# Optimization experiments

Hardware: AMD Instinct MI355X
Metric: run time of the kernel (lower is better)

## Reference

```python
import jax, jax.numpy as jnp
import numpy as np

T = 2048            # context_length
C = 1024            # embedding size
HEAD_QK = 256       # config.head_qk_size
VOCAB = 50257       # config.vocab_size


def setup_inputs() -> dict:
    key = jax.random.key(0)
    k1, k2, k3, k4 = jax.random.split(key, 4)
    x = jax.random.normal(k1, (T, C), dtype=jnp.float32)
    idx = jax.random.randint(k2, (T,), 0, VOCAB, dtype=jnp.int32)
    # Dense kernels (flax Dense stores kernel as [in, out], no bias)
    Wq = jax.random.normal(k3, (C, HEAD_QK), dtype=jnp.float32) / np.sqrt(C)
    Wk = jax.random.normal(k4, (C, HEAD_QK), dtype=jnp.float32) / np.sqrt(C)
    return {"x": x, "idx": idx, "Wq": Wq, "Wk": Wk}


def reference(x, idx, Wq, Wk):
    # q, k: [T, HEAD_QK]
    q = x @ Wq
    k = x @ Wk
    # causal-masked, softmax-free scores: [T, T]
    c = (q @ k.T) * (1.0 / HEAD_QK)
    causal = jnp.tril(jnp.ones((T, T), dtype=bool))
    c = jnp.where(causal, c, 0.0)
    # c @ one_hot(idx, VOCAB) == segment-sum of c's columns by token id
    # out[t, v] = sum_{s : idx[s] == v} c[t, s]   -> [T, VOCAB]
    out = jax.ops.segment_sum(c.T, idx, num_segments=VOCAB).T
    return out
```

## Files before the change

### kernel.cpp

```cpp
#include <hip/hip_runtime.h>

#define T_CTX 2048
#define C_DIM 1024
#define HQK   256
#define NVOC  50257

typedef float nfloat4 __attribute__((ext_vector_type(4)));

__global__ __launch_bounds__(1024) void k_build_first(const int* __restrict__ idx,
                                                      int* __restrict__ first,
                                                      int* __restrict__ vocab_map) {
    __shared__ int sidx[T_CTX];
    __shared__ int skey[4096];
    __shared__ int sval[4096];
    const int tid = threadIdx.x;
    for (int i = tid; i < T_CTX; i += 1024) sidx[i] = idx[i];
    for (int i = tid; i < 4096; i += 1024) { skey[i] = -1; sval[i] = 0x7fffffff; }
    int4* vm4 = reinterpret_cast<int4*>(vocab_map);
    const int4 neg1 = make_int4(-1, -1, -1, -1);
    for (int i = tid; i < 12564; i += 1024) vm4[i] = neg1;
    if (tid == 0) vocab_map[NVOC - 1] = -1;
    __syncthreads();
#pragma unroll
    for (int rep = 0; rep < 2; ++rep) {
        const int s = tid + rep * 1024;
        const int my = sidx[s];
        int h = (int)(((unsigned)my * 2654435761u) >> 16) & 4095;
        while (true) {
            int k = skey[h];
            if (k == my) break;
            if (k == -1) {
                int old = atomicCAS(&skey[h], -1, my);
                if (old == -1 || old == my) break;
            }
            h = (h + 1) & 4095;
        }
        atomicMin(&sval[h], s);
    }
    __syncthreads();
#pragma unroll
    for (int rep = 0; rep < 2; ++rep) {
        const int s = tid + rep * 1024;
        const int my = sidx[s];
        int h = (int)(((unsigned)my * 2654435761u) >> 16) & 4095;
        while (skey[h] != my) h = (h + 1) & 4095;
        const int mp = sval[h];
        first[s] = mp;
        if (mp == s) vocab_map[my] = s;
    }
}

__global__ __launch_bounds__(512) void k_gemm_qk(const float* __restrict__ x,
                                                 const float* __restrict__ Wq,
                                                 const float* __restrict__ Wk,
                                                 float* __restrict__ qbuf,
                                                 float* __restrict__ kT) {
    __shared__ __align__(16) float As[32 * 68];
    __shared__ __align__(16) float Bs[32 * 68];
    const int row0 = blockIdx.x * 64;
    const int col0 = blockIdx.y * 64;
    const bool is_q = (col0 < HQK);
    const float* __restrict__ W = is_q ? Wq : Wk;
    const int wc0 = is_q ? col0 : (col0 - HQK);
    const int tid = threadIdx.x;
    const int tr = (tid >> 4) << 1;
    const int tc = (tid & 15) << 2;
    const int ar = tid >> 3, ak = (tid & 7) << 2;
    const int bk = tid >> 4, bc = (tid & 15) << 2;
    float acc[2][4] = {};
    for (int k0 = 0; k0 < C_DIM; k0 += 32) {
        float4 a4 = *reinterpret_cast<const float4*>(&x[(size_t)(row0 + ar) * C_DIM + k0 + ak]);
        float4 b4 = *reinterpret_cast<const float4*>(&W[(size_t)(k0 + bk) * HQK + wc0 + bc]);
        As[(ak + 0) * 68 + ar] = a4.x; As[(ak + 1) * 68 + ar] = a4.y;
        As[(ak + 2) * 68 + ar] = a4.z; As[(ak + 3) * 68 + ar] = a4.w;
        *reinterpret_cast<float4*>(&Bs[bk * 68 + bc]) = b4;
        __syncthreads();
#pragma unroll
        for (int kk = 0; kk < 32; ++kk) {
            float2 av = *reinterpret_cast<const float2*>(&As[kk * 68 + tr]);
            float4 bv = *reinterpret_cast<const float4*>(&Bs[kk * 68 + tc]);
            const float a[2] = {av.x, av.y};
            const float b[4] = {bv.x, bv.y, bv.z, bv.w};
#pragma unroll
            for (int i = 0; i < 2; ++i)
#pragma unroll
                for (int j = 0; j < 4; ++j) acc[i][j] = fmaf(a[i], b[j], acc[i][j]);
        }
        __syncthreads();
    }
    if (is_q) {
#pragma unroll
        for (int i = 0; i < 2; ++i) {
            float4 o = {acc[i][0], acc[i][1], acc[i][2], acc[i][3]};
            *reinterpret_cast<float4*>(&qbuf[(size_t)(row0 + tr + i) * HQK + col0 + tc]) = o;
        }
    } else {
#pragma unroll
        for (int j = 0; j < 4; ++j) {
            float2 o = {acc[0][j], acc[1][j]};
            *reinterpret_cast<float2*>(&kT[(size_t)(wc0 + tc + j) * T_CTX + row0 + tr]) = o;
        }
    }
}

__global__ __launch_bounds__(512) void k_scores_gemm(const float* __restrict__ q,
                                                     const float* __restrict__ kT,
                                                     float* __restrict__ c) {
    const int bt = blockIdx.x, bs = blockIdx.y;
    if (bs > bt) return;
    __shared__ __align__(16) float As[32 * 68];
    __shared__ __align__(16) float Bs[32 * 68];
    const int row0 = bt * 64;
    const int col0 = bs * 64;
    const int tid = threadIdx.x;
    const int tr = (tid >> 4) << 1;
    const int tc = (tid & 15) << 2;
    const int ar = tid >> 3, ak = (tid & 7) << 2;
    const int bk = tid >> 4, bc = (tid & 15) << 2;
    float acc[2][4] = {};
    for (int k0 = 0; k0 < HQK; k0 += 32) {
        float4 a4 = *reinterpret_cast<const float4*>(&q[(size_t)(row0 + ar) * HQK + k0 + ak]);
        float4 b4 = *reinterpret_cast<const float4*>(&kT[(size_t)(k0 + bk) * T_CTX + col0 + bc]);
        As[(ak + 0) * 68 + ar] = a4.x; As[(ak + 1) * 68 + ar] = a4.y;
        As[(ak + 2) * 68 + ar] = a4.z; As[(ak + 3) * 68 + ar] = a4.w;
        *reinterpret_cast<float4*>(&Bs[bk * 68 + bc]) = b4;
        __syncthreads();
#pragma unroll
        for (int kk = 0; kk < 32; ++kk) {
            float2 av = *reinterpret_cast<const float2*>(&As[kk * 68 + tr]);
            float4 bv = *reinterpret_cast<const float4*>(&Bs[kk * 68 + tc]);
            const float a[2] = {av.x, av.y};
            const float b[4] = {bv.x, bv.y, bv.z, bv.w};
#pragma unroll
            for (int i = 0; i < 2; ++i)
#pragma unroll
                for (int j = 0; j < 4; ++j) acc[i][j] = fmaf(a[i], b[j], acc[i][j]);
        }
        __syncthreads();
    }
    const float scale = 1.0f / 256.0f;
#pragma unroll
    for (int i = 0; i < 2; ++i) {
        float4 o = {acc[i][0] * scale, acc[i][1] * scale, acc[i][2] * scale, acc[i][3] * scale};
        *reinterpret_cast<float4*>(&c[(size_t)(row0 + tr + i) * T_CTX + col0 + tc]) = o;
    }
}

__global__ __launch_bounds__(256) void k_fold_expand(const float* __restrict__ c,
                                                     const int* __restrict__ first,
                                                     const int* __restrict__ vocab_map,
                                                     float* __restrict__ out) {
    __shared__ float rowc[T_CTX];
    const int t = blockIdx.x;
    for (int i = threadIdx.x; i < T_CTX; i += 256) rowc[i] = 0.0f;
    __syncthreads();
    const int nq = (t >> 2) + 1;
    for (int qd = threadIdx.x; qd < nq; qd += 256) {
        const int s0 = qd << 2;
        float4 v = *reinterpret_cast<const float4*>(&c[(size_t)t * T_CTX + s0]);
        int4 f4 = *reinterpret_cast<const int4*>(&first[s0]);
        if (s0 + 3 <= t) {
            atomicAdd(&rowc[f4.x], v.x); atomicAdd(&rowc[f4.y], v.y);
            atomicAdd(&rowc[f4.z], v.z); atomicAdd(&rowc[f4.w], v.w);
        } else {
            atomicAdd(&rowc[f4.x], v.x);
            if (s0 + 1 <= t) atomicAdd(&rowc[f4.y], v.y);
            if (s0 + 2 <= t) atomicAdd(&rowc[f4.z], v.z);
            if (s0 + 3 <= t) atomicAdd(&rowc[f4.w], v.w);
        }
    }
    __syncthreads();
    float* __restrict__ orow = out + (size_t)t * NVOC;
    const int lead = (4 - (t & 3)) & 3;
    if ((int)threadIdx.x < lead) {
        int m = vocab_map[threadIdx.x];
        orow[threadIdx.x] = (m >= 0) ? rowc[m] : 0.0f;
    }
    const int nvec = (NVOC - lead) >> 2;
    for (int i = threadIdx.x; i < nvec; i += 256) {
        const int v = lead + (i << 2);
        int m0 = vocab_map[v + 0], m1 = vocab_map[v + 1];
        int m2 = vocab_map[v + 2], m3 = vocab_map[v + 3];
        nfloat4 o;
        o.x = (m0 >= 0) ? rowc[m0] : 0.0f;
        o.y = (m1 >= 0) ? rowc[m1] : 0.0f;
        o.z = (m2 >= 0) ? rowc[m2] : 0.0f;
        o.w = (m3 >= 0) ? rowc[m3] : 0.0f;
        __builtin_nontemporal_store(o, reinterpret_cast<nfloat4*>(&orow[v]));
    }
    for (int v = lead + (nvec << 2) + threadIdx.x; v < NVOC; v += 256) {
        int m = vocab_map[v];
        orow[v] = (m >= 0) ? rowc[m] : 0.0f;
    }
}

extern "C" void kernel_launch(void* const* d_in, const int* in_sizes, int n_in,
                              void* d_out, int out_size, void* d_ws, size_t ws_size,
                              hipStream_t stream) {
    const float* x   = (const float*)d_in[0];
    const int*   idx = (const int*)d_in[1];
    const float* Wq  = (const float*)d_in[2];
    const float* Wk  = (const float*)d_in[3];
    float* out = (float*)d_out;

    char* ws = (char*)d_ws;
    float* qbuf      = (float*)(ws);
    float* kT        = (float*)(ws + (2u << 20));
    float* c         = (float*)(ws + (4u << 20));
    int*   first     = (int*)(ws + (20u << 20));
    int*   vocab_map = (int*)(ws + (20u << 20) + (16u << 10));

    k_build_first<<<1, 1024, 0, stream>>>(idx, first, vocab_map);
    dim3 gg(32, 8);
    k_gemm_qk<<<gg, 512, 0, stream>>>(x, Wq, Wk, qbuf, kT);
    dim3 gs(32, 32);
    k_scores_gemm<<<gs, 512, 0, stream>>>(qbuf, kT, c);
    k_fold_expand<<<T_CTX, 256, 0, stream>>>(c, first, vocab_map, out);
}
```

Measured before the change: 564.5 us.

## Fold duplicate-token keys into first occurrence before score GEMM, correct causal boundary

Instead of scatter-adding score columns per row with shared atomics, duplicate token columns of kT are summed into their first-occurrence column before the score GEMM. Rows where the causal mask cuts off later duplicates are then fixed by subtracting explicit dot products inside the GEMM epilogue. This makes the expand kernel a plain row copy plus gather, removing the atomic fold. It adds a fold kernel, a separate row-major k buffer, and a per-block loop over all duplicates with syncs, which can be costly if there are many duplicates.

Measured after the change: 588.8 us. +4.3%, slower.

```diff
diff --git a/kernel.cpp b/kernel.cpp
--- a/kernel.cpp
+++ b/kernel.cpp
@@ -9,17 +9,21 @@
 
 __global__ __launch_bounds__(1024) void k_build_first(const int* __restrict__ idx,
                                                       int* __restrict__ first,
-                                                      int* __restrict__ vocab_map) {
+                                                      int* __restrict__ vocab_map,
+                                                      int* __restrict__ ndup_g,
+                                                      int* __restrict__ dup_s,
+                                                      int* __restrict__ dup_f) {
     __shared__ int sidx[T_CTX];
     __shared__ int skey[4096];
     __shared__ int sval[4096];
+    __shared__ int sndup;
     const int tid = threadIdx.x;
     for (int i = tid; i < T_CTX; i += 1024) sidx[i] = idx[i];
     for (int i = tid; i < 4096; i += 1024) { skey[i] = -1; sval[i] = 0x7fffffff; }
     int4* vm4 = reinterpret_cast<int4*>(vocab_map);
     const int4 neg1 = make_int4(-1, -1, -1, -1);
     for (int i = tid; i < 12564; i += 1024) vm4[i] = neg1;
-    if (tid == 0) vocab_map[NVOC - 1] = -1;
+    if (tid == 0) { vocab_map[NVOC - 1] = -1; sndup = 0; }
     __syncthreads();
 #pragma unroll
     for (int rep = 0; rep < 2; ++rep) {
@@ -46,15 +50,23 @@
         while (skey[h] != my) h = (h + 1) & 4095;
         const int mp = sval[h];
         first[s] = mp;
-        if (mp == s) vocab_map[my] = s;
-    }
+        if (mp == s) {
+            vocab_map[my] = s;
+        } else {
+            int p = atomicAdd(&sndup, 1);
+            dup_s[p] = s; dup_f[p] = mp;
+        }
+    }
+    __syncthreads();
+    if (tid == 0) ndup_g[0] = sndup;
 }
 
 __global__ __launch_bounds__(512) void k_gemm_qk(const float* __restrict__ x,
                                                  const float* __restrict__ Wq,
                                                  const float* __restrict__ Wk,
                                                  float* __restrict__ qbuf,
-                                                 float* __restrict__ kT) {
+                                                 float* __restrict__ kT,
+                                                 float* __restrict__ kbuf) {
     __shared__ __align__(16) float As[32 * 68];
     __shared__ __align__(16) float Bs[32 * 68];
     const int row0 = blockIdx.x * 64;
@@ -100,19 +112,45 @@
             float2 o = {acc[0][j], acc[1][j]};
             *reinterpret_cast<float2*>(&kT[(size_t)(wc0 + tc + j) * T_CTX + row0 + tr]) = o;
         }
+#pragma unroll
+        for (int i = 0; i < 2; ++i) {
+            float4 o = {acc[i][0], acc[i][1], acc[i][2], acc[i][3]};
+            *reinterpret_cast<float4*>(&kbuf[(size_t)(row0 + tr + i) * HQK + wc0 + tc]) = o;
+        }
+    }
+}
+
+__global__ __launch_bounds__(256) void k_foldk(float* __restrict__ kT,
+                                               const int* __restrict__ ndup_g,
+                                               const int* __restrict__ dup_s,
+                                               const int* __restrict__ dup_f) {
+    const int nd = ndup_g[0];
+    const int total = nd * HQK;
+    for (int j = blockIdx.x * 256 + threadIdx.x; j < total; j += gridDim.x * 256) {
+        const int e = j >> 8, d = j & 255;
+        atomicAdd(&kT[(size_t)d * T_CTX + dup_f[e]], kT[(size_t)d * T_CTX + dup_s[e]]);
     }
 }
 
 __global__ __launch_bounds__(512) void k_scores_gemm(const float* __restrict__ q,
                                                      const float* __restrict__ kT,
-                                                     float* __restrict__ c) {
+                                                     const float* __restrict__ kbuf,
+                                                     const int* __restrict__ ndup_g,
+                                                     const int* __restrict__ dup_s,
+                                                     const int* __restrict__ dup_f,
+                                                     float* __restrict__ out_c) {
     const int bt = blockIdx.x, bs = blockIdx.y;
     if (bs > bt) return;
     __shared__ __align__(16) float As[32 * 68];
     __shared__ __align__(16) float Bs[32 * 68];
+    __shared__ int sds[2048];
+    __shared__ int sdf[2048];
+    __shared__ float skv[HQK];
     const int row0 = bt * 64;
     const int col0 = bs * 64;
     const int tid = threadIdx.x;
+    const int nd = ndup_g[0];
+    for (int i = tid; i < nd; i += 512) { sds[i] = dup_s[i]; sdf[i] = dup_f[i]; }
     const int tr = (tid >> 4) << 1;
     const int tc = (tid & 15) << 2;
     const int ar = tid >> 3, ak = (tid & 7) << 2;
@@ -139,42 +177,56 @@
         __syncthreads();
     }
     const float scale = 1.0f / 256.0f;
+    for (int e = 0; e < nd; ++e) {
+        const int f = sdf[e], s2 = sds[e];
+        const int tlo = (f > row0) ? f : row0;
+        const int thi = (s2 - 1 < row0 + 63) ? (s2 - 1) : (row0 + 63);
+        if (f < col0 || f >= col0 + 64 || tlo > thi) continue;
+        __syncthreads();
+        if (tid < 64) {
+            float4 kv = *reinterpret_cast<const float4*>(&kbuf[(size_t)s2 * HQK + tid * 4]);
+            *reinterpret_cast<float4*>(&skv[tid * 4]) = kv;
+        }
+        __syncthreads();
+        const int jf = f - col0 - tc;
+        if (jf >= 0 && jf < 4) {
+#pragma unroll
+            for (int i = 0; i < 2; ++i) {
+                const int t = row0 + tr + i;
+                if (t >= tlo && t <= thi) {
+                    float dot = 0.0f;
+                    const float4* qp = reinterpret_cast<const float4*>(&q[(size_t)t * HQK]);
+#pragma unroll 8
+                    for (int d4 = 0; d4 < 64; ++d4) {
+                        float4 qv = qp[d4];
+                        dot = fmaf(qv.x, skv[d4 * 4 + 0], fmaf(qv.y, skv[d4 * 4 + 1],
+                              fmaf(qv.z, skv[d4 * 4 + 2], fmaf(qv.w, skv[d4 * 4 + 3], dot))));
+                    }
+#pragma unroll
+                    for (int jj = 0; jj < 4; ++jj) if (jj == jf) acc[i][jj] -= dot;
+                }
+            }
+        }
+    }
 #pragma unroll
     for (int i = 0; i < 2; ++i) {
         float4 o = {acc[i][0] * scale, acc[i][1] * scale, acc[i][2] * scale, acc[i][3] * scale};
-        *reinterpret_cast<float4*>(&c[(size_t)(row0 + tr + i) * T_CTX + col0 + tc]) = o;
-    }
-}
-
-__global__ __launch_bounds__(256) void k_fold_expand(const float* __restrict__ c,
-                                                     const int* __restrict__ first,
-                                                     const int* __restrict__ vocab_map,
-                                                     float* __restrict__ out) {
+        *reinterpret_cast<float4*>(&out_c[(size_t)(row0 + tr + i) * T_CTX + col0 + tc]) = o;
+    }
+}
+
+__global__ __launch_bounds__(256) void k_expand(const float* __restrict__ out_c,
+                                                const int* __restrict__ vocab_map,
+                                                float* __restrict__ out) {
     __shared__ float rowc[T_CTX];
     const int t = blockIdx.x;
-    for (int i = threadIdx.x; i < T_CTX; i += 256) rowc[i] = 0.0f;
-    __syncthreads();
-    const int nq = (t >> 2) + 1;
-    for (int qd = threadIdx.x; qd < nq; qd += 256) {
-        const int s0 = qd << 2;
-        float4 v = *reinterpret_cast<const float4*>(&c[(size_t)t * T_CTX + s0]);
-        int4 f4 = *reinterpret_cast<const int4*>(&first[s0]);
-        if (s0 + 3 <= t) {
-            atomicAdd(&rowc[f4.x], v.x); atomicAdd(&rowc[f4.y], v.y);
-            atomicAdd(&rowc[f4.z], v.z); atomicAdd(&rowc[f4.w], v.w);
-        } else {
-            atomicAdd(&rowc[f4.x], v.x);
-            if (s0 + 1 <= t) atomicAdd(&rowc[f4.y], v.y);
-            if (s0 + 2 <= t) atomicAdd(&rowc[f4.z], v.z);
-            if (s0 + 3 <= t) atomicAdd(&rowc[f4.w], v.w);
-        }
-    }
+    for (int i = threadIdx.x; i < T_CTX; i += 256) rowc[i] = out_c[(size_t)t * T_CTX + i];
     __syncthreads();
     float* __restrict__ orow = out + (size_t)t * NVOC;
     const int lead = (4 - (t & 3)) & 3;
     if ((int)threadIdx.x < lead) {
         int m = vocab_map[threadIdx.x];
-        orow[threadIdx.x] = (m >= 0) ? rowc[m] : 0.0f;
+        orow[threadIdx.x] = (m >= 0 && m <= t) ? rowc[m] : 0.0f;
     }
     const int nvec = (NVOC - lead) >> 2;
     for (int i = threadIdx.x; i < nvec; i += 256) {
@@ -182,15 +234,15 @@
         int m0 = vocab_map[v + 0], m1 = vocab_map[v + 1];
         int m2 = vocab_map[v + 2], m3 = vocab_map[v + 3];
         nfloat4 o;
-        o.x = (m0 >= 0) ? rowc[m0] : 0.0f;
-        o.y = (m1 >= 0) ? rowc[m1] : 0.0f;
-        o.z = (m2 >= 0) ? rowc[m2] : 0.0f;
-        o.w = (m3 >= 0) ? rowc[m3] : 0.0f;
+        o.x = (m0 >= 0 && m0 <= t) ? rowc[m0] : 0.0f;
+        o.y = (m1 >= 0 && m1 <= t) ? rowc[m1] : 0.0f;
+        o.z = (m2 >= 0 && m2 <= t) ? rowc[m2] : 0.0f;
+        o.w = (m3 >= 0 && m3 <= t) ? rowc[m3] : 0.0f;
         __builtin_nontemporal_store(o, reinterpret_cast<nfloat4*>(&orow[v]));
     }
     for (int v = lead + (nvec << 2) + threadIdx.x; v < NVOC; v += 256) {
         int m = vocab_map[v];
-        orow[v] = (m >= 0) ? rowc[m] : 0.0f;
+        orow[v] = (m >= 0 && m <= t) ? rowc[m] : 0.0f;
     }
 }
 
@@ -206,14 +258,19 @@
     char* ws = (char*)d_ws;
     float* qbuf      = (float*)(ws);
     float* kT        = (float*)(ws + (2u << 20));
-    float* c         = (float*)(ws + (4u << 20));
-    int*   first     = (int*)(ws + (20u << 20));
-    int*   vocab_map = (int*)(ws + (20u << 20) + (16u << 10));
-
-    k_build_first<<<1, 1024, 0, stream>>>(idx, first, vocab_map);
+    float* kbuf      = (float*)(ws + (4u << 20));
+    float* out_c     = (float*)(ws + (6u << 20));
+    int*   first     = (int*)(ws + (22u << 20));
+    int*   vocab_map = (int*)(ws + (22u << 20) + (16u << 10));
+    int*   ndup_g    = (int*)(ws + (23u << 20));
+    int*   dup_s     = (int*)(ws + (23u << 20) + 64);
+    int*   dup_f     = (int*)(ws + (23u << 20) + 64 + (8u << 10));
+
+    k_build_first<<<1, 1024, 0, stream>>>(idx, first, vocab_map, ndup_g, dup_s, dup_f);
     dim3 gg(32, 8);
-    k_gemm_qk<<<gg, 512, 0, stream>>>(x, Wq, Wk, qbuf, kT);
+    k_gemm_qk<<<gg, 512, 0, stream>>>(x, Wq, Wk, qbuf, kT, kbuf);
+    k_foldk<<<64, 256, 0, stream>>>(kT, ndup_g, dup_s, dup_f);
     dim3 gs(32, 32);
-    k_scores_gemm<<<gs, 512, 0, stream>>>(qbuf, kT, c);
-    k_fold_expand<<<T_CTX, 256, 0, stream>>>(c, first, vocab_map, out);
-}
+    k_scores_gemm<<<gs, 512, 0, stream>>>(qbuf, kT, kbuf, ndup_g, dup_s, dup_f, out_c);
+    k_expand<<<T_CTX, 256, 0, stream>>>(out_c, vocab_map, out);
+}
```
